# Kernel optimization log

Hardware: AMD Instinct MI355X
Metric: run time of the kernel (lower is better)

## Reference

```python
import jax, jax.numpy as jnp
import numpy as np

M_TOKENS = 8192
IN_F = 4096
OUT_F = 4096


def setup_inputs() -> dict:
    key = jax.random.key(0)
    k1, k2, k3, k4, k5 = jax.random.split(key, 5)
    x = jax.random.normal(k1, (M_TOKENS, IN_F), dtype=jnp.float32)
    # int8-range quantized weight, stored as int32 (values in [0, 255) like uint8 reinterpretation)
    w_q = jax.random.randint(k2, (OUT_F, IN_F), 0, 255, dtype=jnp.int32)
    scale = jax.random.uniform(k3, (OUT_F,), dtype=jnp.float32, minval=0.001, maxval=0.02)
    zero_point = jax.random.uniform(k4, (OUT_F,), dtype=jnp.float32, minval=0.0, maxval=128.0)
    bias = jax.random.normal(k5, (OUT_F,), dtype=jnp.float32)
    return {"x": x, "w_q": w_q, "scale": scale, "zero_point": zero_point, "bias": bias}


def reference(x, w_q, scale, zero_point, bias):
    # Per-channel (axis=0 / out_features) dequantization: w = (q - zp) * s
    w = (w_q.astype(jnp.float32) - zero_point[:, None]) * scale[:, None]  # [out, in]
    # F.linear: y = x @ w.T + b
    return jnp.einsum('mi,oi->mo', x, w) + bias
```

## Files before the change

### kernel.cpp

```cpp
#include <hip/hip_runtime.h>


typedef unsigned char u8;
typedef signed char s8;
typedef __attribute__((ext_vector_type(4))) int i32x4;
typedef __attribute__((ext_vector_type(4))) float f32x4;

#define M_TOK 8192
#define KDIM 4096
#define NDIM 4096
#define NT (KDIM / 64)


__device__ __forceinline__ int pack4(int a, int b, int c, int d) {
  return (a & 255) | ((b & 255) << 8) | ((c & 255) << 16) |
         (int)(((unsigned)(d & 255)) << 24);
}

#define GLDS(gptr, lptr)                                                      \
  __builtin_amdgcn_global_load_lds(                                          \
      (const __attribute__((address_space(1))) void*)(gptr),                 \
      (__attribute__((address_space(3))) void*)(lptr), 16, 0, 0)


__global__ __launch_bounds__(256) void convert_x_kernel(
    const float* __restrict__ x, s8* __restrict__ xq,
    float* __restrict__ sx, float* __restrict__ rq) {
  const int row = blockIdx.x;
  const int tid = threadIdx.x;
  const float* xr = x + (size_t)row * KDIM + tid * 16;
  float4 v[4];
#pragma unroll
  for (int i = 0; i < 4; ++i) v[i] = ((const float4*)xr)[i];

  float mx = 0.f;
#pragma unroll
  for (int i = 0; i < 4; ++i) {
    mx = fmaxf(mx, fabsf(v[i].x)); mx = fmaxf(mx, fabsf(v[i].y));
    mx = fmaxf(mx, fabsf(v[i].z)); mx = fmaxf(mx, fabsf(v[i].w));
  }
#pragma unroll
  for (int off = 32; off > 0; off >>= 1)
    mx = fmaxf(mx, __shfl_down(mx, off, 64));
  __shared__ float redf[4];
  __shared__ float bmax;
  if ((tid & 63) == 0) redf[tid >> 6] = mx;
  __syncthreads();
  if (tid == 0)
    bmax = fmaxf(fmaxf(redf[0], redf[1]), fmaxf(redf[2], redf[3]));
  __syncthreads();
  const float maxv = bmax;
  const float inv = 127.0f / fmaxf(maxv, 1e-30f);

  int q[16];
  int ssum = 0;
#pragma unroll
  for (int i = 0; i < 4; ++i) {
    q[i * 4 + 0] = (int)rintf(v[i].x * inv);
    q[i * 4 + 1] = (int)rintf(v[i].y * inv);
    q[i * 4 + 2] = (int)rintf(v[i].z * inv);
    q[i * 4 + 3] = (int)rintf(v[i].w * inv);
  }
#pragma unroll
  for (int i = 0; i < 16; ++i) ssum += q[i];

  int4 o;
  o.x = pack4(q[0], q[1], q[2], q[3]);
  o.y = pack4(q[4], q[5], q[6], q[7]);
  o.z = pack4(q[8], q[9], q[10], q[11]);
  o.w = pack4(q[12], q[13], q[14], q[15]);
  *(int4*)(xq + (size_t)row * KDIM + tid * 16) = o;

#pragma unroll
  for (int off = 32; off > 0; off >>= 1) ssum += __shfl_down(ssum, off, 64);
  __shared__ int redi[4];
  if ((tid & 63) == 0) redi[tid >> 6] = ssum;
  __syncthreads();
  if (tid == 0) {
    sx[row] = maxv * (1.0f / 127.0f);
    rq[row] = (float)(redi[0] + redi[1] + redi[2] + redi[3]);
  }
}


__global__ __launch_bounds__(256) void convert_w_kernel(
    const int* __restrict__ wq, s8* __restrict__ wb) {
  const size_t idx = (size_t)blockIdx.x * 256 + threadIdx.x;
  const int4* src = (const int4*)wq + idx * 4;
  const int4 a = src[0], b = src[1], c = src[2], d = src[3];
  int4 o;
  o.x = pack4(a.x - 128, a.y - 128, a.z - 128, a.w - 128);
  o.y = pack4(b.x - 128, b.y - 128, b.z - 128, b.w - 128);
  o.z = pack4(c.x - 128, c.y - 128, c.z - 128, c.w - 128);
  o.w = pack4(d.x - 128, d.y - 128, d.z - 128, d.w - 128);
  ((int4*)wb)[idx] = o;
}


__global__ __launch_bounds__(512, 2) void qlin_gemm_kernel(
    const u8* __restrict__ A,
    const u8* __restrict__ B,
    const float* __restrict__ sx,
    const float* __restrict__ rq,
    const float* __restrict__ scale,
    const float* __restrict__ zp,
    const float* __restrict__ bias,
    float* __restrict__ out) {
  extern __shared__ u8 lds[];
  u8* Al = lds;
  u8* Bl = lds + 32768;

  const int tid = threadIdx.x;
  const int lane = tid & 63;
  const int wave = tid >> 6;
  const int wm = wave >> 2;
  const int wn = wave & 3;

  const int bid = blockIdx.x;
  const int swz = (bid & 7) * 64 + (bid >> 3);
  const int bm = swz >> 4;
  const int bn = swz & 15;
  const int row0 = bm * 256, col0 = bn * 256;

  const int fr = lane & 15;
  const int fk = lane >> 4;
  const u8* Ags = A + (size_t)(row0 + wave * 16 + fr) * KDIM + fk * 16;
  const u8* Bgs = B + (size_t)(col0 + wave * 16 + fr) * KDIM + fk * 16;
  u8* AldW = Al + wave * 1024;
  u8* BldW = Bl + wave * 1024;

#define STAGE_A(d, tau, h)                                                    \
  GLDS(Ags + (size_t)(h) * 128 * KDIM + (tau) * 64,                          \
       AldW + (d) * 16384 + (h) * 8192)
#define STAGE_B(d, tau, h)                                                    \
  GLDS(Bgs + (size_t)(h) * 128 * KDIM + (tau) * 64,                          \
       BldW + (d) * 16384 + (h) * 8192)

  const u8* ArL = Al + wm * 8192 + lane * 16;
  const u8* BrL = Bl + (wn >> 1) * 8192 + (wn & 1) * 4096 + lane * 16;

#define LDA(d, m) (*(const i32x4*)(ArL + (d) * 16384 + (m) * 1024))
#define LDB(d, n) (*(const i32x4*)(BrL + (d) * 16384 + (n) * 1024))
#define MFMA(d, va, vb) \
  d = __builtin_amdgcn_mfma_i32_16x16x64_i8(va, vb, d, 0, 0, 0)

  i32x4 acc[8][4] = {};
  i32x4 a[8], b[4];

  STAGE_A(0, 0, 0); STAGE_A(0, 0, 1);
  STAGE_B(0, 0, 0); STAGE_B(0, 0, 1);
  STAGE_A(1, 1, 0); STAGE_A(1, 1, 1);
  asm volatile("s_waitcnt vmcnt(2)" ::: "memory");
  __builtin_amdgcn_s_barrier();
#pragma unroll
  for (int m = 0; m < 4; ++m) a[m] = LDA(0, m);

  for (int t = 0; t < NT; ++t) {
    const int d = t & 1;

    b[0] = LDB(d, 0); b[1] = LDB(d, 1);
    asm volatile("" ::: "memory");
    b[2] = LDB(d, 2); b[3] = LDB(d, 3);
    if (t + 1 < NT) STAGE_B(d ^ 1, t + 1, 0);
    __builtin_amdgcn_s_barrier();
    asm volatile("s_waitcnt lgkmcnt(2)" ::: "memory");
    __builtin_amdgcn_s_setprio(1);
#pragma unroll
    for (int m = 0; m < 4; ++m)
#pragma unroll
      for (int n = 0; n < 2; ++n) MFMA(acc[m][n], a[m], b[n]);
    __builtin_amdgcn_s_setprio(0);
    __builtin_amdgcn_s_barrier();

#pragma unroll
    for (int m = 4; m < 8; ++m) a[m] = LDA(d, m);
    if (t + 1 < NT) STAGE_B(d ^ 1, t + 1, 1);
    __builtin_amdgcn_s_barrier();
    asm volatile("s_waitcnt lgkmcnt(4)" ::: "memory");
    __builtin_amdgcn_s_setprio(1);
#pragma unroll
    for (int m = 0; m < 4; ++m)
#pragma unroll
      for (int n = 2; n < 4; ++n) MFMA(acc[m][n], a[m], b[n]);
    __builtin_amdgcn_s_setprio(0);
    __builtin_amdgcn_s_barrier();

    if (t + 1 < NT) {
      asm volatile("s_waitcnt vmcnt(2)" ::: "memory");
    }
    __builtin_amdgcn_s_barrier();
    asm volatile("s_waitcnt lgkmcnt(0)" ::: "memory");
    __builtin_amdgcn_s_setprio(1);
#pragma unroll
    for (int m = 4; m < 8; ++m)
#pragma unroll
      for (int n = 0; n < 2; ++n) MFMA(acc[m][n], a[m], b[n]);
    __builtin_amdgcn_s_setprio(0);
    __builtin_amdgcn_s_barrier();

    if (t + 1 < NT) {
#pragma unroll
      for (int m = 0; m < 4; ++m) a[m] = LDA(d ^ 1, m);
    }
    if (t + 2 < NT) { STAGE_A(d, t + 2, 0); STAGE_A(d, t + 2, 1); }
    __builtin_amdgcn_s_barrier();
    __builtin_amdgcn_s_setprio(1);
#pragma unroll
    for (int m = 4; m < 8; ++m)
#pragma unroll
      for (int n = 2; n < 4; ++n) MFMA(acc[m][n], a[m], b[n]);
    __builtin_amdgcn_s_setprio(0);
    if (t < NT - 2) {
      asm volatile("s_waitcnt vmcnt(2)" ::: "memory");
    } else {
      asm volatile("s_waitcnt vmcnt(0)" ::: "memory");
    }
    __builtin_amdgcn_s_barrier();
  }

  {
    const int wrow0 = row0 + wm * 128;
    const int wcol0 = col0 + wn * 64;
    float* eps = (float*)lds + wave * 1088;
    const f32x4 p4 = *(const f32x4*)(scale + wcol0 + 4 * fr);
    const f32x4 z4 = *(const f32x4*)(zp + wcol0 + 4 * fr);
    const f32x4 b4 = *(const f32x4*)(bias + wcol0 + 4 * fr);
    const f32x4 w04 = p4 * (128.0f - z4);
#pragma unroll
    for (int c = 0; c < 8; ++c) {
#pragma unroll
      for (int n = 0; n < 4; ++n)
#pragma unroll
        for (int q = 0; q < 4; ++q)
          eps[(fk * 4 + q) * 68 + n * 16 + fr] = (float)acc[c][n][q];
      asm volatile("s_waitcnt lgkmcnt(0)" ::: "memory");
#pragma unroll
      for (int j = 0; j < 4; ++j) {
        const int rl = j * 4 + fk;
        const int grow = wrow0 + c * 16 + rl;
        const f32x4 v = *(const f32x4*)(eps + rl * 68 + 4 * fr);
        const float sxr = sx[grow];
        const float rqr = rq[grow];
        const f32x4 o4 = sxr * (p4 * v + w04 * rqr) + b4;
        *(f32x4*)(out + (size_t)grow * NDIM + wcol0 + 4 * fr) = o4;
      }
      asm volatile("s_waitcnt lgkmcnt(0)" ::: "memory");
    }
  }
#undef STAGE_A
#undef STAGE_B
#undef LDA
#undef LDB
#undef MFMA
}


extern "C" void kernel_launch(void* const* d_in, const int* in_sizes, int n_in,
                              void* d_out, int out_size, void* d_ws,
                              size_t ws_size, hipStream_t stream) {
  const float* x = (const float*)d_in[0];
  const int* wq = (const int*)d_in[1];
  const float* scale = (const float*)d_in[2];
  const float* zp = (const float*)d_in[3];
  const float* bias = (const float*)d_in[4];
  float* out = (float*)d_out;

  char* ws = (char*)d_ws;
  s8* xq = (s8*)ws;
  s8* wq8 = (s8*)(ws + (size_t)M_TOK * KDIM);
  float* sx = (float*)(ws + (size_t)M_TOK * KDIM + (size_t)NDIM * KDIM);
  float* rq = (float*)(ws + (size_t)M_TOK * KDIM + (size_t)NDIM * KDIM +
                       (size_t)M_TOK * 4);

  (void)hipFuncSetAttribute((const void*)qlin_gemm_kernel,
                            hipFuncAttributeMaxDynamicSharedMemorySize,
                            65536);

  convert_x_kernel<<<M_TOK, 256, 0, stream>>>(x, xq, sx, rq);
  convert_w_kernel<<<(NDIM * (size_t)KDIM) / (256 * 16), 256, 0, stream>>>(
      wq, wq8);

  qlin_gemm_kernel<<<dim3((M_TOK / 256) * (NDIM / 256)), dim3(512), 65536,
                     stream>>>((const u8*)xq, (const u8*)wq8, sx, rq, scale,
                               zp, bias, out);
}
```

Before: 198.1 us.

## Shrink GEMM tile to 256x128 with 4 waves and XOR-swizzled LDS staging

The int8 GEMM block moves from a 256x256 tile with 8 waves to a 256x128 tile with 4 waves, each wave computing 128x64. LDS use drops to 48KB and the grid doubles. Staging rows are written with an XOR swizzle on the 16-byte slot so fragment reads from LDS avoid bank conflicts. The per-K-step schedule is cut from four MFMA phases with many barriers to two phases, with all A fragments loaded up front. The risk is lower data reuse per tile, since B is read twice as often, and a coarser load/compute overlap.

```diff
diff --git a/kernel.cpp b/kernel.cpp
--- a/kernel.cpp
+++ b/kernel.cpp
@@ -97,7 +97,7 @@
 }
 
 
-__global__ __launch_bounds__(512, 2) void qlin_gemm_kernel(
+__global__ __launch_bounds__(256, 2) void qlin_gemm_kernel(
     const u8* __restrict__ A,
     const u8* __restrict__ B,
     const float* __restrict__ sx,
@@ -113,105 +113,85 @@
   const int tid = threadIdx.x;
   const int lane = tid & 63;
   const int wave = tid >> 6;
-  const int wm = wave >> 2;
-  const int wn = wave & 3;
+  const int wm = wave >> 1;
+  const int wn = wave & 1;
 
   const int bid = blockIdx.x;
-  const int swz = (bid & 7) * 64 + (bid >> 3);
-  const int bm = swz >> 4;
-  const int bn = swz & 15;
-  const int row0 = bm * 256, col0 = bn * 256;
+  const int swz = (bid & 7) * 128 + (bid >> 3);
+  const int bm = swz >> 5;
+  const int bn = swz & 31;
+  const int row0 = bm * 256, col0 = bn * 128;
+
+  const int srow = lane >> 2;
+  const int sslot = (lane & 3) ^ (srow & 3);
+  const u8* Ags = A + (size_t)(row0 + wave * 64 + srow) * KDIM + sslot * 16;
+  const u8* Bgs = B + (size_t)(col0 + wave * 32 + srow) * KDIM + sslot * 16;
+  u8* AldW = Al + wave * 4096;
+  u8* BldW = Bl + wave * 2048;
+
+#define STAGE_A(d, tau)                                                       \
+  do {                                                                        \
+    _Pragma("unroll") for (int i = 0; i < 4; ++i)                             \
+        GLDS(Ags + (size_t)i * 16 * KDIM + (size_t)(tau) * 64,               \
+             AldW + (d) * 16384 + i * 1024);                                 \
+  } while (0)
+
+#define STAGE_B(d, tau)                                                       \
+  do {                                                                        \
+    _Pragma("unroll") for (int j = 0; j < 2; ++j)                             \
+        GLDS(Bgs + (size_t)j * 16 * KDIM + (size_t)(tau) * 64,               \
+             BldW + (d) * 8192 + j * 1024);                                  \
+  } while (0)
 
   const int fr = lane & 15;
-  const int fk = lane >> 4;
-  const u8* Ags = A + (size_t)(row0 + wave * 16 + fr) * KDIM + fk * 16;
-  const u8* Bgs = B + (size_t)(col0 + wave * 16 + fr) * KDIM + fk * 16;
-  u8* AldW = Al + wave * 1024;
-  u8* BldW = Bl + wave * 1024;
-
-#define STAGE_A(d, tau, h)                                                    \
-  GLDS(Ags + (size_t)(h) * 128 * KDIM + (tau) * 64,                          \
-       AldW + (d) * 16384 + (h) * 8192)
-#define STAGE_B(d, tau, h)                                                    \
-  GLDS(Bgs + (size_t)(h) * 128 * KDIM + (tau) * 64,                          \
-       BldW + (d) * 16384 + (h) * 8192)
-
-  const u8* ArL = Al + wm * 8192 + lane * 16;
-  const u8* BrL = Bl + (wn >> 1) * 8192 + (wn & 1) * 4096 + lane * 16;
-
-#define LDA(d, m) (*(const i32x4*)(ArL + (d) * 16384 + (m) * 1024))
-#define LDB(d, n) (*(const i32x4*)(BrL + (d) * 16384 + (n) * 1024))
+  const int g = lane >> 4;
+  const int sw = ((g ^ (fr & 3)) << 4);
+  const u8* Ar = Al + (wm * 128 + fr) * 64 + sw;
+  const u8* Br = Bl + (wn * 64 + fr) * 64 + sw;
+
+#define LDA(d, m) (*(const i32x4*)(Ar + (d) * 16384 + (m) * 1024))
+#define LDB(d, n) (*(const i32x4*)(Br + (d) * 8192 + (n) * 1024))
 #define MFMA(d, va, vb) \
   d = __builtin_amdgcn_mfma_i32_16x16x64_i8(va, vb, d, 0, 0, 0)
 
   i32x4 acc[8][4] = {};
   i32x4 a[8], b[4];
 
-  STAGE_A(0, 0, 0); STAGE_A(0, 0, 1);
-  STAGE_B(0, 0, 0); STAGE_B(0, 0, 1);
-  STAGE_A(1, 1, 0); STAGE_A(1, 1, 1);
-  asm volatile("s_waitcnt vmcnt(2)" ::: "memory");
+  STAGE_A(0, 0);
+  STAGE_B(0, 0);
+  STAGE_A(1, 1);
+  asm volatile("s_waitcnt vmcnt(4)" ::: "memory");
   __builtin_amdgcn_s_barrier();
-#pragma unroll
-  for (int m = 0; m < 4; ++m) a[m] = LDA(0, m);
 
   for (int t = 0; t < NT; ++t) {
     const int d = t & 1;
 
+#pragma unroll
+    for (int m = 0; m < 8; ++m) a[m] = LDA(d, m);
     b[0] = LDB(d, 0); b[1] = LDB(d, 1);
     asm volatile("" ::: "memory");
     b[2] = LDB(d, 2); b[3] = LDB(d, 3);
-    if (t + 1 < NT) STAGE_B(d ^ 1, t + 1, 0);
-    __builtin_amdgcn_s_barrier();
+    if (t + 1 < NT) STAGE_B(d ^ 1, t + 1);
     asm volatile("s_waitcnt lgkmcnt(2)" ::: "memory");
     __builtin_amdgcn_s_setprio(1);
 #pragma unroll
-    for (int m = 0; m < 4; ++m)
+    for (int m = 0; m < 8; ++m)
 #pragma unroll
       for (int n = 0; n < 2; ++n) MFMA(acc[m][n], a[m], b[n]);
     __builtin_amdgcn_s_setprio(0);
+
+    asm volatile("s_waitcnt lgkmcnt(0)" ::: "memory");
     __builtin_amdgcn_s_barrier();
-
-#pragma unroll
-    for (int m = 4; m < 8; ++m) a[m] = LDA(d, m);
-    if (t + 1 < NT) STAGE_B(d ^ 1, t + 1, 1);
-    __builtin_amdgcn_s_barrier();
-    asm volatile("s_waitcnt lgkmcnt(4)" ::: "memory");
+    if (t + 2 < NT) STAGE_A(d, t + 2);
     __builtin_amdgcn_s_setprio(1);
 #pragma unroll
-    for (int m = 0; m < 4; ++m)
+    for (int m = 0; m < 8; ++m)
 #pragma unroll
       for (int n = 2; n < 4; ++n) MFMA(acc[m][n], a[m], b[n]);
     __builtin_amdgcn_s_setprio(0);
-    __builtin_amdgcn_s_barrier();
-
-    if (t + 1 < NT) {
-      asm volatile("s_waitcnt vmcnt(2)" ::: "memory");
-    }
-    __builtin_amdgcn_s_barrier();
-    asm volatile("s_waitcnt lgkmcnt(0)" ::: "memory");
-    __builtin_amdgcn_s_setprio(1);
-#pragma unroll
-    for (int m = 4; m < 8; ++m)
-#pragma unroll
-      for (int n = 0; n < 2; ++n) MFMA(acc[m][n], a[m], b[n]);
-    __builtin_amdgcn_s_setprio(0);
-    __builtin_amdgcn_s_barrier();
-
-    if (t + 1 < NT) {
-#pragma unroll
-      for (int m = 0; m < 4; ++m) a[m] = LDA(d ^ 1, m);
-    }
-    if (t + 2 < NT) { STAGE_A(d, t + 2, 0); STAGE_A(d, t + 2, 1); }
-    __builtin_amdgcn_s_barrier();
-    __builtin_amdgcn_s_setprio(1);
-#pragma unroll
-    for (int m = 4; m < 8; ++m)
-#pragma unroll
-      for (int n = 2; n < 4; ++n) MFMA(acc[m][n], a[m], b[n]);
-    __builtin_amdgcn_s_setprio(0);
+
     if (t < NT - 2) {
-      asm volatile("s_waitcnt vmcnt(2)" ::: "memory");
+      asm volatile("s_waitcnt vmcnt(4)" ::: "memory");
     } else {
       asm volatile("s_waitcnt vmcnt(0)" ::: "memory");
     }
@@ -221,23 +201,26 @@
   {
     const int wrow0 = row0 + wm * 128;
     const int wcol0 = col0 + wn * 64;
-    float* eps = (float*)lds + wave * 1088;
+    float* eps = (float*)lds + wave * 2176;
     const f32x4 p4 = *(const f32x4*)(scale + wcol0 + 4 * fr);
     const f32x4 z4 = *(const f32x4*)(zp + wcol0 + 4 * fr);
     const f32x4 b4 = *(const f32x4*)(bias + wcol0 + 4 * fr);
     const f32x4 w04 = p4 * (128.0f - z4);
 #pragma unroll
-    for (int c = 0; c < 8; ++c) {
-#pragma unroll
-      for (int n = 0; n < 4; ++n)
-#pragma unroll
-        for (int q = 0; q < 4; ++q)
-          eps[(fk * 4 + q) * 68 + n * 16 + fr] = (float)acc[c][n][q];
+    for (int c = 0; c < 4; ++c) {
+#pragma unroll
+      for (int mm = 0; mm < 2; ++mm)
+#pragma unroll
+        for (int n = 0; n < 4; ++n)
+#pragma unroll
+          for (int q = 0; q < 4; ++q)
+            eps[(mm * 16 + g * 4 + q) * 68 + n * 16 + fr] =
+                (float)acc[2 * c + mm][n][q];
       asm volatile("s_waitcnt lgkmcnt(0)" ::: "memory");
 #pragma unroll
-      for (int j = 0; j < 4; ++j) {
-        const int rl = j * 4 + fk;
-        const int grow = wrow0 + c * 16 + rl;
+      for (int j = 0; j < 8; ++j) {
+        const int rl = j * 4 + g;
+        const int grow = wrow0 + c * 32 + rl;
         const f32x4 v = *(const f32x4*)(eps + rl * 68 + 4 * fr);
         const float sxr = sx[grow];
         const float rqr = rq[grow];
@@ -274,13 +257,13 @@
 
   (void)hipFuncSetAttribute((const void*)qlin_gemm_kernel,
                             hipFuncAttributeMaxDynamicSharedMemorySize,
-                            65536);
+                            49152);
 
   convert_x_kernel<<<M_TOK, 256, 0, stream>>>(x, xq, sx, rq);
   convert_w_kernel<<<(NDIM * (size_t)KDIM) / (256 * 16), 256, 0, stream>>>(
       wq, wq8);
 
-  qlin_gemm_kernel<<<dim3((M_TOK / 256) * (NDIM / 256)), dim3(512), 65536,
+  qlin_gemm_kernel<<<dim3((M_TOK / 256) * (NDIM / 128)), dim3(256), 49152,
                      stream>>>((const u8*)xq, (const u8*)wq8, sx, rq, scale,
                                zp, bias, out);
 }
```

After: 190.4 us. -3.9%, faster.
